# Kernel tuning notes

Measured on AMD Instinct MI355X. Metric: run time of the kernel, lower is better.

The kernel has to match this reference:

```python
import jax, jax.numpy as jnp
import numpy as np

NEG_SLOPE = 0.2
NUM_GRAPHS = 64


def _gat_layer(x, src, dst, W, att_src, att_dst, bias, concat):
    # x: [N, Fin]; W: [Fin, H*C]; att_*: [H, C]; bias: [H*C] or [C]
    N = x.shape[0]
    H, C = att_src.shape
    h = (x @ W).reshape(N, H, C)                      # per-head projections
    a_src = jnp.sum(h * att_src, axis=-1)             # [N, H]
    a_dst = jnp.sum(h * att_dst, axis=-1)             # [N, H]
    e = jax.nn.leaky_relu(a_src[src] + a_dst[dst], NEG_SLOPE)  # [E, H]
    # segment softmax over incoming edges per destination node
    m = jnp.full((N, H), -jnp.inf, dtype=e.dtype).at[dst].max(e)
    p = jnp.exp(e - m[dst])                           # [E, H]
    denom = jnp.zeros((N, H), dtype=e.dtype).at[dst].add(p)
    alpha = p / denom[dst]                            # [E, H]
    msg = h[src] * alpha[:, :, None]                  # [E, H, C]
    out = jnp.zeros((N, H, C), dtype=h.dtype).at[dst].add(msg)
    out = out.reshape(N, H * C) if concat else out.mean(axis=1)
    return out + bias


def _with_self_loops(edge_index, n):
    loop = jnp.arange(n, dtype=edge_index.dtype)
    src = jnp.concatenate([edge_index[0], loop])
    dst = jnp.concatenate([edge_index[1], loop])
    return src, dst


def setup_inputs() -> dict:
    key = jax.random.key(0)
    ks = jax.random.split(key, 12)
    N, E, Fin, C, H, A = 50000, 800000, 128, 64, 4, 32
    HC = H * C
    x = jax.random.normal(ks[0], (N, Fin), dtype=jnp.float32)
    edge_index = jax.random.randint(ks[1], (2, E), 0, N, dtype=jnp.int64)
    batch = jnp.sort(jax.random.randint(ks[2], (N,), 0, NUM_GRAPHS, dtype=jnp.int64))
    s1 = 1.0 / np.sqrt(Fin)
    s2 = 1.0 / np.sqrt(HC)
    return {
        "x": x,
        "edge_index": edge_index,
        "batch": batch,
        "num_wires": 8,
        "num_terminals": 8,
        "W1": jax.random.normal(ks[3], (Fin, HC), dtype=jnp.float32) * s1,
        "att_src1": jax.random.normal(ks[4], (H, C), dtype=jnp.float32) * s1,
        "att_dst1": jax.random.normal(ks[5], (H, C), dtype=jnp.float32) * s1,
        "b1": jnp.zeros((HC,), dtype=jnp.float32),
        "W2": jax.random.normal(ks[6], (HC, HC), dtype=jnp.float32) * s2,
        "att_src2": jax.random.normal(ks[7], (H, C), dtype=jnp.float32) * s2,
        "att_dst2": jax.random.normal(ks[8], (H, C), dtype=jnp.float32) * s2,
        "b2": jnp.zeros((C,), dtype=jnp.float32),
        "Wa": jax.random.normal(ks[9], (C, A), dtype=jnp.float32) * (1.0 / np.sqrt(C)),
        "ba": jnp.zeros((A,), dtype=jnp.float32),
    }


def reference(x, edge_index, batch, num_wires, num_terminals,
              W1, att_src1, att_dst1, b1, W2, att_src2, att_dst2, b2, Wa, ba):
    N = x.shape[0]
    src, dst = _with_self_loops(edge_index, N)
    h = jax.nn.elu(_gat_layer(x, src, dst, W1, att_src1, att_dst1, b1, concat=True))
    h = jax.nn.elu(_gat_layer(h, src, dst, W2, att_src2, att_dst2, b2, concat=False))
    # global mean pool per graph
    sums = jax.ops.segment_sum(h, batch, num_segments=NUM_GRAPHS)
    cnts = jax.ops.segment_sum(jnp.ones((N,), dtype=h.dtype), batch, num_segments=NUM_GRAPHS)
    pooled = sums / jnp.maximum(cnts, 1.0)[:, None]   # [G, C]
    return pooled @ Wa + ba                            # [G, num_actions]
```

## Files before the change

### kernel.cpp

```cpp
#include <hip/hip_runtime.h>
#include <hip/hip_bf16.h>
#include <cstdint>
#include <cstddef>

#define FIN      128
#define HGAT_H   4
#define HGAT_C   64
#define HGAT_HC  256
#define NGRAPHS  64
#define NACT     32
#define LOG2E    1.4426950408889634f

typedef unsigned int   uint32;
typedef unsigned short ushort_t;

using short8 = __attribute__((ext_vector_type(8))) short;
using u16x8  = __attribute__((ext_vector_type(8))) ushort_t;
using f32x4  = __attribute__((ext_vector_type(4))) float;
using f32x2  = __attribute__((ext_vector_type(2))) float;

__device__ __forceinline__ float bf2f(ushort_t u) {
    return __uint_as_float(((uint32)u) << 16);
}
__device__ __forceinline__ float bflo(uint32 q) {
    return __uint_as_float(q << 16);
}
__device__ __forceinline__ float bfhi(uint32 q) {
    return __uint_as_float(q & 0xFFFF0000u);
}
__device__ __forceinline__ ushort_t f2bf(float f) {
    __hip_bfloat16 h = __float2bfloat16(f);
    return *reinterpret_cast<ushort_t*>(&h);
}

__device__ __forceinline__ void att_fold_one(
    const float* __restrict__ W, const float* __restrict__ as,
    const float* __restrict__ ad, ushort_t* __restrict__ attBt,
    int K, int idx)
{
    const int k = idx >> 3, j = idx & 7;
    const int h = j >> 1;
    const float* av = (j & 1) ? ad : as;
    float s = 0.f;
#pragma unroll 8
    for (int c = 0; c < HGAT_C; ++c)
        s += W[(size_t)k * HGAT_HC + h * 64 + c] * av[h * 64 + c];
    const ushort_t hi = f2bf(s);
    const float    lo = s - bf2f(hi);
    attBt[(size_t)j * K + k]       = hi;
    attBt[(size_t)(j + 8) * K + k] = f2bf(lo);
}

#define CNT_BLOCKS 128

__global__ __launch_bounds__(256) void bucket_count_prep_kernel(
    const int* __restrict__ ei, int* __restrict__ bcnt,
    const float* __restrict__ W1, const float* __restrict__ W2,
    const float* __restrict__ as1, const float* __restrict__ ad1,
    const float* __restrict__ as2, const float* __restrict__ ad2,
    ushort_t* __restrict__ Wt1, ushort_t* __restrict__ Wt2,
    ushort_t* __restrict__ attBt1, ushort_t* __restrict__ attBt2, int E)
{
    const int t = threadIdx.x;
    if (blockIdx.x < CNT_BLOCKS) {
        __shared__ int hist[256];
        hist[t] = 0;
        __syncthreads();
        const int chunk = (E + CNT_BLOCKS - 1) / CNT_BLOCKS;
        const int lo = blockIdx.x * chunk;
        const int hi = min(lo + chunk, E);
        for (int e = lo + t; e < hi; e += 256)
            atomicAdd(&hist[ei[E + e] >> 8], 1);
        __syncthreads();
        if (hist[t] > 0) atomicAdd(&bcnt[t], hist[t]);
        return;
    }
    const int idx = (blockIdx.x - CNT_BLOCKS) * 256 + t;
    const int n1 = FIN * HGAT_HC;
    const int n2 = HGAT_HC * HGAT_HC;
    if (idx < n1) {
        const int k = idx >> 8, c = idx & 255;
        Wt1[(size_t)c * FIN + k] = f2bf(W1[idx]);
    } else if (idx < n1 + n2) {
        const int j = idx - n1;
        const int k = j >> 8, c = j & 255;
        Wt2[(size_t)c * HGAT_HC + k] = f2bf(W2[j]);
    } else if (idx < n1 + n2 + FIN * 8) {
        att_fold_one(W1, as1, ad1, attBt1, FIN, idx - n1 - n2);
    } else if (idx < n1 + n2 + (FIN + HGAT_HC) * 8) {
        att_fold_one(W2, as2, ad2, attBt2, HGAT_HC, idx - n1 - n2 - FIN * 8);
    }
}

__global__ __launch_bounds__(256) void bucket_scan_kernel(
    const int* __restrict__ bcnt, int* __restrict__ boff,
    int* __restrict__ bcur)
{
    __shared__ int sm[256];
    const int t = threadIdx.x;
    const int v = bcnt[t];
    sm[t] = v;
    __syncthreads();
#pragma unroll
    for (int off = 1; off < 256; off <<= 1) {
        const int u = (t >= off) ? sm[t - off] : 0;
        __syncthreads();
        sm[t] += u;
        __syncthreads();
    }
    const int ex = sm[t] - v;
    boff[t] = ex;
    bcur[t] = ex;
    if (t == 255) boff[256] = sm[255];
}

__global__ __launch_bounds__(256) void bucket_scatter_kernel(
    const int* __restrict__ ei, int* __restrict__ bcur,
    int2* __restrict__ staging, int E)
{
    __shared__ int hist[256];
    __shared__ int base[256];
    __shared__ int cur[256];
    const int t = threadIdx.x;
    hist[t] = 0;
    __syncthreads();

    const int chunk = 4096;
    const int lo = blockIdx.x * chunk;
    const int hi = min(lo + chunk, E);

    for (int e = lo + t; e < hi; e += 256)
        atomicAdd(&hist[ei[E + e] >> 8], 1);
    __syncthreads();
    if (hist[t] > 0) base[t] = atomicAdd(&bcur[t], hist[t]);
    cur[t] = 0;
    __syncthreads();

    for (int e = lo + t; e < hi; e += 256) {
        const int s = ei[e];
        const int d = ei[E + e];
        const int b = d >> 8;
        const int r = atomicAdd(&cur[b], 1);
        staging[base[b] + r] = make_int2(s, d);
    }
}

__global__ __launch_bounds__(256) void bucket_fill_kernel(
    const int2* __restrict__ staging, const int* __restrict__ boff,
    int* __restrict__ rowptr, int* __restrict__ colsrc, int N, int E)
{
    __shared__ int deg[256];
    __shared__ int ssc[256];
    __shared__ int cur[256];
    const int t  = threadIdx.x;
    const int b  = blockIdx.x;
    const int lo = boff[b];
    const int hi = boff[b + 1];

    deg[t] = 0;
    __syncthreads();
    for (int e = lo + t; e < hi; e += 256)
        atomicAdd(&deg[staging[e].y & 255], 1);
    __syncthreads();

    const int v = deg[t];
    ssc[t] = v;
    __syncthreads();
#pragma unroll
    for (int off = 1; off < 256; off <<= 1) {
        const int u = (t >= off) ? ssc[t - off] : 0;
        __syncthreads();
        ssc[t] += u;
        __syncthreads();
    }
    const int pre  = ssc[t] - v;
    const int node = b * 256 + t;
    if (node < N) rowptr[node] = lo + pre;
    cur[t] = lo + pre;
    if (b == 0 && t == 0) rowptr[N] = E;
    __syncthreads();

    for (int e = lo + t; e < hi; e += 256) {
        const int2 sd = staging[e];
        const int pos = atomicAdd(&cur[sd.y & 255], 1);
        colsrc[pos] = sd.x;
    }
}

template <int K, bool AF32>
__global__ __launch_bounds__(256) void gemm_mfma_att_kernel(
    const void* __restrict__ Av, const ushort_t* __restrict__ Bt,
    const ushort_t* __restrict__ attBt, ushort_t* __restrict__ Cb,
    float* __restrict__ a_src, float* __restrict__ a_dst, int M)
{
    constexpr int KK   = K / 32;
    constexpr int NPF  = K / 32;
    constexpr int BSTR = K + 8;
    constexpr int CSTR = 72;
    __shared__ ushort_t Bs[64 * BSTR];
    __shared__ ushort_t AttS[16 * BSTR];
    __shared__ ushort_t Cs[64 * CSTR];

    const int t  = threadIdx.x;
    const int w  = t >> 6;
    const int l  = t & 63;
    const int lg = l >> 4;
    const int lr = l & 15;
    const int rowbase = blockIdx.x * 64 + w * 16;

    const int srow  = t & 63;
    const int cbase = (t >> 6) * (K / 4);

    short8 af[KK];
    {
        const int arow = rowbase + lr;
        const int gr   = arow < M ? arow : M - 1;
        if (AF32) {
            const float* Ap = (const float*)Av + (size_t)gr * K;
#pragma unroll
            for (int kk = 0; kk < KK; ++kk) {
                const float4 v0 = *reinterpret_cast<const float4*>(Ap + kk * 32 + lg * 8);
                const float4 v1 = *reinterpret_cast<const float4*>(Ap + kk * 32 + lg * 8 + 4);
                short8 s;
                s[0] = (short)f2bf(v0.x); s[1] = (short)f2bf(v0.y);
                s[2] = (short)f2bf(v0.z); s[3] = (short)f2bf(v0.w);
                s[4] = (short)f2bf(v1.x); s[5] = (short)f2bf(v1.y);
                s[6] = (short)f2bf(v1.z); s[7] = (short)f2bf(v1.w);
                af[kk] = s;
            }
        } else {
            const ushort_t* Ap = (const ushort_t*)Av + (size_t)gr * K;
#pragma unroll
            for (int kk = 0; kk < KK; ++kk)
                af[kk] = *reinterpret_cast<const short8*>(Ap + kk * 32 + lg * 8);
        }
    }

    {
        const int r  = t & 15;
        const int cb = (t >> 4) * (K / 16);
        const ushort_t* src = attBt + (size_t)r * K + cb;
        ushort_t*       dst = &AttS[r * BSTR + cb];
#pragma unroll
        for (int j = 0; j < K / 128; ++j)
            *reinterpret_cast<u16x8*>(dst + j * 8) =
                *reinterpret_cast<const u16x8*>(src + j * 8);
    }
    {
        const ushort_t* src = Bt + (size_t)srow * K + cbase;
        ushort_t*       dst = &Bs[srow * BSTR + cbase];
#pragma unroll
        for (int j = 0; j < NPF; ++j)
            *reinterpret_cast<u16x8*>(dst + j * 8) =
                *reinterpret_cast<const u16x8*>(src + j * 8);
    }
    __syncthreads();

    {
        f32x4 aacc = {0.f, 0.f, 0.f, 0.f};
#pragma unroll
        for (int kk = 0; kk < KK; ++kk) {
            const short8 bfr = *reinterpret_cast<const short8*>(
                &AttS[lr * BSTR + kk * 32 + lg * 8]);
            aacc = __builtin_amdgcn_mfma_f32_16x16x32_bf16(af[kk], bfr, aacc, 0, 0, 0);
        }
#pragma unroll
        for (int reg = 0; reg < 4; ++reg) {
            const int gm = rowbase + lg * 4 + reg;
            const float v = aacc[reg] + __shfl_xor(aacc[reg], 8);
            if (lr < 8 && gm < M) {
                const int hh = lr >> 1;
                if (lr & 1) a_dst[gm * 4 + hh] = v * LOG2E;
                else        a_src[gm * 4 + hh] = v * LOG2E;
            }
        }
    }

    u16x8 pf[NPF];
#pragma unroll
    for (int head = 0; head < HGAT_H; ++head) {
        if (head < HGAT_H - 1) {
            const ushort_t* src =
                Bt + ((size_t)(head + 1) * 64 + srow) * K + cbase;
#pragma unroll
            for (int j = 0; j < NPF; ++j)
                pf[j] = *reinterpret_cast<const u16x8*>(src + j * 8);
        }

        f32x4 acc[4];
#pragma unroll
        for (int ct = 0; ct < 4; ++ct) acc[ct] = {0.f, 0.f, 0.f, 0.f};

#pragma unroll
        for (int kk = 0; kk < KK; ++kk) {
            short8 bfr[4];
#pragma unroll
            for (int ct = 0; ct < 4; ++ct)
                bfr[ct] = *reinterpret_cast<const short8*>(
                    &Bs[(ct * 16 + lr) * BSTR + kk * 32 + lg * 8]);
#pragma unroll
            for (int ct = 0; ct < 4; ++ct)
                acc[ct] = __builtin_amdgcn_mfma_f32_16x16x32_bf16(
                    af[kk], bfr[ct], acc[ct], 0, 0, 0);
        }

#pragma unroll
        for (int reg = 0; reg < 4; ++reg) {
            const int r = w * 16 + lg * 4 + reg;
#pragma unroll
            for (int ct = 0; ct < 4; ++ct)
                Cs[r * CSTR + ct * 16 + lr] = f2bf(acc[ct][reg]);
        }
        __syncthreads();

        const int n0 = head * 64;
        {
            const int cc = (t & 7) * 8;
#pragma unroll
            for (int it = 0; it < 2; ++it) {
                const int r  = (t >> 3) + it * 32;
                const int gm = blockIdx.x * 64 + r;
                if (gm < M) {
                    const u16x8 val = *reinterpret_cast<const u16x8*>(&Cs[r * CSTR + cc]);
                    *reinterpret_cast<u16x8*>(&Cb[(size_t)gm * HGAT_HC + n0 + cc]) = val;
                }
            }
        }

        if (head < HGAT_H - 1) {
            ushort_t* dst = &Bs[srow * BSTR + cbase];
#pragma unroll
            for (int j = 0; j < NPF; ++j)
                *reinterpret_cast<u16x8*>(dst + j * 8) = pf[j];
        }
        __syncthreads();
    }
}

template <int MODE>
__global__ __launch_bounds__(256) void aggregate_csr_kernel(
    const int* __restrict__ rowptr, const int* __restrict__ colsrc,
    const ushort_t* __restrict__ hb, const float* __restrict__ a_src,
    const float* __restrict__ a_dst, const float* __restrict__ bias,
    ushort_t* __restrict__ out, int N)
{
    const int wave = (blockIdx.x * 256 + threadIdx.x) >> 6;
    const int lane = threadIdx.x & 63;
    const int half = lane >> 5;
    const int hl   = lane & 31;
    const int d    = wave * 2 + half;
    if (d >= N) return;

    const int c0 = hl * 8;
    const int h  = hl >> 3;
    const float ad = a_dst[d * 4 + h];

    f32x2 a01 = {0.f, 0.f}, a23 = {0.f, 0.f}, a45 = {0.f, 0.f}, a67 = {0.f, 0.f};
    float den = 0.f;

    const int beg = rowptr[d], end = rowptr[d + 1];
    int i = beg;
    for (; i + 4 <= end; i += 4) {
        int   sv[4];
        float av[4];
        uint4 qv[4];
#pragma unroll
        for (int j = 0; j < 4; ++j) sv[j] = colsrc[i + j];
#pragma unroll
        for (int j = 0; j < 4; ++j) av[j] = a_src[sv[j] * 4 + h];
#pragma unroll
        for (int j = 0; j < 4; ++j)
            qv[j] = *reinterpret_cast<const uint4*>(&hb[(size_t)sv[j] * HGAT_HC + c0]);
#pragma unroll
        for (int j = 0; j < 4; ++j) {
            float ee = av[j] + ad;
            ee = fmaxf(ee, 0.2f * ee);
            const float wgt = __builtin_amdgcn_exp2f(ee);
            const f32x2 w2 = {wgt, wgt};
            a01 += w2 * f32x2{bflo(qv[j].x), bfhi(qv[j].x)};
            a23 += w2 * f32x2{bflo(qv[j].y), bfhi(qv[j].y)};
            a45 += w2 * f32x2{bflo(qv[j].z), bfhi(qv[j].z)};
            a67 += w2 * f32x2{bflo(qv[j].w), bfhi(qv[j].w)};
            den += wgt;
        }
    }
    for (; i < end; ++i) {
        const int s = colsrc[i];
        float ee = a_src[s * 4 + h] + ad;
        ee = fmaxf(ee, 0.2f * ee);
        const float wgt = __builtin_amdgcn_exp2f(ee);
        const uint4 q = *reinterpret_cast<const uint4*>(&hb[(size_t)s * HGAT_HC + c0]);
        const f32x2 w2 = {wgt, wgt};
        a01 += w2 * f32x2{bflo(q.x), bfhi(q.x)};
        a23 += w2 * f32x2{bflo(q.y), bfhi(q.y)};
        a45 += w2 * f32x2{bflo(q.z), bfhi(q.z)};
        a67 += w2 * f32x2{bflo(q.w), bfhi(q.w)};
        den += wgt;
    }
    {
        float ee = a_src[d * 4 + h] + ad;
        ee = fmaxf(ee, 0.2f * ee);
        const float wgt = __builtin_amdgcn_exp2f(ee);
        const uint4 q = *reinterpret_cast<const uint4*>(&hb[(size_t)d * HGAT_HC + c0]);
        const f32x2 w2 = {wgt, wgt};
        a01 += w2 * f32x2{bflo(q.x), bfhi(q.x)};
        a23 += w2 * f32x2{bflo(q.y), bfhi(q.y)};
        a45 += w2 * f32x2{bflo(q.z), bfhi(q.z)};
        a67 += w2 * f32x2{bflo(q.w), bfhi(q.w)};
        den += wgt;
    }

    const float inv = 1.0f / den;
    float v[8] = {a01.x * inv, a01.y * inv, a23.x * inv, a23.y * inv,
                  a45.x * inv, a45.y * inv, a67.x * inv, a67.y * inv};

    if (MODE == 0) {
        const float4 b0 = *reinterpret_cast<const float4*>(&bias[c0]);
        const float4 b1 = *reinterpret_cast<const float4*>(&bias[c0 + 4]);
        v[0] += b0.x; v[1] += b0.y; v[2] += b0.z; v[3] += b0.w;
        v[4] += b1.x; v[5] += b1.y; v[6] += b1.z; v[7] += b1.w;
        u16x8 u;
#pragma unroll
        for (int j = 0; j < 8; ++j) {
            const float r = v[j] > 0.f ? v[j] : expm1f(v[j]);
            u[j] = f2bf(r);
        }
        *reinterpret_cast<u16x8*>(&out[(size_t)d * HGAT_HC + c0]) = u;
    } else {
#pragma unroll
        for (int j = 0; j < 8; ++j) {
            v[j] += __shfl_xor(v[j], 8);
            v[j] += __shfl_xor(v[j], 16);
        }
        if (hl < 8) {
            const int c = hl * 8;
            const float4 b0 = *reinterpret_cast<const float4*>(&bias[c]);
            const float4 b1 = *reinterpret_cast<const float4*>(&bias[c + 4]);
            const float bb[8] = {b0.x, b0.y, b0.z, b0.w, b1.x, b1.y, b1.z, b1.w};
            u16x8 u;
#pragma unroll
            for (int j = 0; j < 8; ++j) {
                float r = 0.25f * v[j] + bb[j];
                r = r > 0.f ? r : expm1f(r);
                u[j] = f2bf(r);
            }
            *reinterpret_cast<u16x8*>(&out[(size_t)d * HGAT_C + c]) = u;
        }
    }
}

__device__ __forceinline__ int lower_bound_batch(
    const int* __restrict__ batch, int N, int key)
{
    int lo = 0, hi = N;
    while (lo < hi) {
        const int mid = (lo + hi) >> 1;
        if (batch[mid] < key) lo = mid + 1; else hi = mid;
    }
    return lo;
}

__global__ __launch_bounds__(256) void pool_partial_kernel(
    const ushort_t* __restrict__ hfin, const int* __restrict__ batch,
    float* __restrict__ partial, int N)
{
    const int g   = blockIdx.x >> 3;
    const int s   = blockIdx.x & 7;
    const int t   = threadIdx.x;
    const int c   = t & 63;
    const int sub = t >> 6;

    const int beg = lower_bound_batch(batch, N, g);
    const int end = lower_bound_batch(batch, N, g + 1);
    const int len = end - beg;
    const int sl  = (len + 7) >> 3;
    const int sb  = beg + s * sl;
    const int se  = sb + sl < end ? sb + sl : end;

    float acc = 0.f;
    for (int n = sb + sub; n < se; n += 4)
        acc += bf2f(hfin[(size_t)n * HGAT_C + c]);

    __shared__ float sm[256];
    sm[t] = acc;
    __syncthreads();
    if (sub == 0)
        partial[(size_t)(g * 8 + s) * HGAT_C + c] =
            sm[c] + sm[64 + c] + sm[128 + c] + sm[192 + c];
}

__global__ __launch_bounds__(64) void pool_final_fused_kernel(
    const float* __restrict__ partial, const int* __restrict__ batch,
    const float* __restrict__ Wa, const float* __restrict__ ba,
    float* __restrict__ out, int N)
{
    const int g = blockIdx.x;
    const int c = threadIdx.x;
    const int beg = lower_bound_batch(batch, N, g);
    const int end = lower_bound_batch(batch, N, g + 1);
    float s = 0.f;
#pragma unroll
    for (int k = 0; k < 8; ++k)
        s += partial[(size_t)(g * 8 + k) * HGAT_C + c];
    s /= fmaxf((float)(end - beg), 1.0f);

    __shared__ float pr[HGAT_C];
    pr[c] = s;
    __syncthreads();
    if (c < NACT) {
        float o = ba[c];
#pragma unroll
        for (int cc = 0; cc < HGAT_C; ++cc)
            o += pr[cc] * Wa[cc * NACT + c];
        out[g * NACT + c] = o;
    }
}

extern "C" void kernel_launch(void* const* d_in, const int* in_sizes, int n_in,
                              void* d_out, int out_size, void* d_ws, size_t ws_size,
                              hipStream_t stream)
{
    const float* x     = (const float*)d_in[0];
    const int*   ei    = (const int*)d_in[1];
    const int*   batch = (const int*)d_in[2];
    const float* W1    = (const float*)d_in[5];
    const float* as1   = (const float*)d_in[6];
    const float* ad1   = (const float*)d_in[7];
    const float* b1    = (const float*)d_in[8];
    const float* W2    = (const float*)d_in[9];
    const float* as2   = (const float*)d_in[10];
    const float* ad2   = (const float*)d_in[11];
    const float* b2    = (const float*)d_in[12];
    const float* Wa    = (const float*)d_in[13];
    const float* ba    = (const float*)d_in[14];

    const int N = in_sizes[0] / FIN;
    const int E = in_sizes[1] / 2;

    char* ws = (char*)d_ws;
    size_t off = 0;
    auto alloc = [&](size_t bytes) -> void* {
        void* p = ws + off;
        off += (bytes + 255) & ~(size_t)255;
        return p;
    };
    ushort_t* hb      = (ushort_t*)alloc((size_t)N * HGAT_HC * 2);
    ushort_t* hpost   = (ushort_t*)alloc((size_t)N * HGAT_HC * 2);
    ushort_t* Wt1     = (ushort_t*)alloc((size_t)FIN * HGAT_HC * 2);
    ushort_t* Wt2     = (ushort_t*)alloc((size_t)HGAT_HC * HGAT_HC * 2);
    ushort_t* attBt1  = (ushort_t*)alloc((size_t)16 * FIN * 2);
    ushort_t* attBt2  = (ushort_t*)alloc((size_t)16 * HGAT_HC * 2);
    float*    a_src   = (float*)alloc((size_t)N * 4 * 4);
    float*    a_dst   = (float*)alloc((size_t)N * 4 * 4);
    int*      rowptr  = (int*)alloc((size_t)(N + 1) * 4);
    int*      colsrc  = (int*)alloc((size_t)E * 4);
    int2*     staging = (int2*)alloc((size_t)E * 8);
    int*      bcnt    = (int*)alloc(256 * 4);
    int*      boff    = (int*)alloc(257 * 4);
    int*      bcur    = (int*)alloc(256 * 4);
    float*    partial = (float*)alloc((size_t)NGRAPHS * 8 * HGAT_C * 4);
    ushort_t* hfin    = hpost;
    (void)ws_size; (void)n_in; (void)out_size;

    const int gemmBlocks = (N + 63) / 64;
    const int aggBlocks  = (N + 7) / 8;
    const int NBKT       = (N + 255) >> 8;
    const int prepTot    = FIN * HGAT_HC + HGAT_HC * HGAT_HC + (FIN + HGAT_HC) * 8;
    const int prepBlocks = (prepTot + 255) / 256;

    hipMemsetAsync(bcnt, 0, 256 * 4, stream);
    bucket_count_prep_kernel<<<CNT_BLOCKS + prepBlocks, 256, 0, stream>>>(
        ei, bcnt, W1, W2, as1, ad1, as2, ad2, Wt1, Wt2, attBt1, attBt2, E);
    bucket_scan_kernel<<<1, 256, 0, stream>>>(bcnt, boff, bcur);
    bucket_scatter_kernel<<<(E + 4095) / 4096, 256, 0, stream>>>(
        ei, bcur, staging, E);
    bucket_fill_kernel<<<NBKT, 256, 0, stream>>>(
        staging, boff, rowptr, colsrc, N, E);

    gemm_mfma_att_kernel<FIN, true><<<gemmBlocks, 256, 0, stream>>>(
        x, Wt1, attBt1, hb, a_src, a_dst, N);
    aggregate_csr_kernel<0><<<aggBlocks, 256, 0, stream>>>(
        rowptr, colsrc, hb, a_src, a_dst, b1, hpost, N);

    gemm_mfma_att_kernel<HGAT_HC, false><<<gemmBlocks, 256, 0, stream>>>(
        hpost, Wt2, attBt2, hb, a_src, a_dst, N);
    aggregate_csr_kernel<1><<<aggBlocks, 256, 0, stream>>>(
        rowptr, colsrc, hb, a_src, a_dst, b2, hfin, N);

    pool_partial_kernel<<<NGRAPHS * 8, 256, 0, stream>>>(hfin, batch, partial, N);
    pool_final_fused_kernel<<<NGRAPHS, 64, 0, stream>>>(
        partial, batch, Wa, ba, (float*)d_out, N);
}
```

Baseline: 238.9 us.

## Fuse edge scatter with first GEMM launch and replace atomic bucket count

Each counting block now writes its own 256-bin histogram to a per-block array, and the scan kernel reduces those in a loop. This removes the memset and the global atomics. The bucket scatter and the first-layer projection GEMM are merged into one launch with block-index dispatch, so the memory-bound scatter blocks can run alongside the MFMA GEMM blocks and one launch is saved. The cost is a serial 128-step reduction per thread in the scan kernel. The fused kernel's shared memory and register use is set by the larger GEMM body, which can limit how many scatter blocks fit per CU.

Result: faster. 225.8 us (median of 2 runs) (-5.5%).

```diff
diff --git a/kernel.cpp b/kernel.cpp
--- a/kernel.cpp
+++ b/kernel.cpp
@@ -10,6 +10,7 @@
 #define NGRAPHS  64
 #define NACT     32
 #define LOG2E    1.4426950408889634f
+#define CNT_BLOCKS 128
 
 typedef unsigned int   uint32;
 typedef unsigned short ushort_t;
@@ -51,10 +52,8 @@
     attBt[(size_t)(j + 8) * K + k] = f2bf(lo);
 }
 
-#define CNT_BLOCKS 128
-
 __global__ __launch_bounds__(256) void bucket_count_prep_kernel(
-    const int* __restrict__ ei, int* __restrict__ bcnt,
+    const int* __restrict__ ei, int* __restrict__ bhist,
     const float* __restrict__ W1, const float* __restrict__ W2,
     const float* __restrict__ as1, const float* __restrict__ ad1,
     const float* __restrict__ as2, const float* __restrict__ ad2,
@@ -72,7 +71,7 @@
         for (int e = lo + t; e < hi; e += 256)
             atomicAdd(&hist[ei[E + e] >> 8], 1);
         __syncthreads();
-        if (hist[t] > 0) atomicAdd(&bcnt[t], hist[t]);
+        bhist[blockIdx.x * 256 + t] = hist[t];
         return;
     }
     const int idx = (blockIdx.x - CNT_BLOCKS) * 256 + t;
@@ -93,12 +92,13 @@
 }
 
 __global__ __launch_bounds__(256) void bucket_scan_kernel(
-    const int* __restrict__ bcnt, int* __restrict__ boff,
+    const int* __restrict__ bhist, int* __restrict__ boff,
     int* __restrict__ bcur)
 {
     __shared__ int sm[256];
     const int t = threadIdx.x;
-    const int v = bcnt[t];
+    int v = 0;
+    for (int j = 0; j < CNT_BLOCKS; ++j) v += bhist[j * 256 + t];
     sm[t] = v;
     __syncthreads();
 #pragma unroll
@@ -114,9 +114,9 @@
     if (t == 255) boff[256] = sm[255];
 }
 
-__global__ __launch_bounds__(256) void bucket_scatter_kernel(
+__device__ __forceinline__ void scatter_body(
     const int* __restrict__ ei, int* __restrict__ bcur,
-    int2* __restrict__ staging, int E)
+    int2* __restrict__ staging, int E, int blk)
 {
     __shared__ int hist[256];
     __shared__ int base[256];
@@ -126,7 +126,7 @@
     __syncthreads();
 
     const int chunk = 4096;
-    const int lo = blockIdx.x * chunk;
+    const int lo = blk * chunk;
     const int hi = min(lo + chunk, E);
 
     for (int e = lo + t; e < hi; e += 256)
@@ -188,10 +188,10 @@
 }
 
 template <int K, bool AF32>
-__global__ __launch_bounds__(256) void gemm_mfma_att_kernel(
+__device__ __forceinline__ void gemm_body(
     const void* __restrict__ Av, const ushort_t* __restrict__ Bt,
     const ushort_t* __restrict__ attBt, ushort_t* __restrict__ Cb,
-    float* __restrict__ a_src, float* __restrict__ a_dst, int M)
+    float* __restrict__ a_src, float* __restrict__ a_dst, int M, int blk)
 {
     constexpr int KK   = K / 32;
     constexpr int NPF  = K / 32;
@@ -206,7 +206,7 @@
     const int l  = t & 63;
     const int lg = l >> 4;
     const int lr = l & 15;
-    const int rowbase = blockIdx.x * 64 + w * 16;
+    const int rowbase = blk * 64 + w * 16;
 
     const int srow  = t & 63;
     const int cbase = (t >> 6) * (K / 4);
@@ -319,7 +319,7 @@
 #pragma unroll
             for (int it = 0; it < 2; ++it) {
                 const int r  = (t >> 3) + it * 32;
-                const int gm = blockIdx.x * 64 + r;
+                const int gm = blk * 64 + r;
                 if (gm < M) {
                     const u16x8 val = *reinterpret_cast<const u16x8*>(&Cs[r * CSTR + cc]);
                     *reinterpret_cast<u16x8*>(&Cb[(size_t)gm * HGAT_HC + n0 + cc]) = val;
@@ -335,6 +335,29 @@
         }
         __syncthreads();
     }
+}
+
+__global__ __launch_bounds__(256) void scatter_gemm1_kernel(
+    const int* __restrict__ ei, int* __restrict__ bcur,
+    int2* __restrict__ staging, int E, int SB,
+    const float* __restrict__ x, const ushort_t* __restrict__ Wt1,
+    const ushort_t* __restrict__ attBt1, ushort_t* __restrict__ hb,
+    float* __restrict__ a_src, float* __restrict__ a_dst, int M)
+{
+    if ((int)blockIdx.x < SB) {
+        scatter_body(ei, bcur, staging, E, blockIdx.x);
+        return;
+    }
+    gemm_body<FIN, true>(x, Wt1, attBt1, hb, a_src, a_dst, M,
+                         blockIdx.x - SB);
+}
+
+__global__ __launch_bounds__(256) void gemm2_kernel(
+    const ushort_t* __restrict__ A, const ushort_t* __restrict__ Wt2,
+    const ushort_t* __restrict__ attBt2, ushort_t* __restrict__ hb,
+    float* __restrict__ a_src, float* __restrict__ a_dst, int M)
+{
+    gemm_body<HGAT_HC, false>(A, Wt2, attBt2, hb, a_src, a_dst, M, blockIdx.x);
 }
 
 template <int MODE>
@@ -555,7 +578,7 @@
     int*      rowptr  = (int*)alloc((size_t)(N + 1) * 4);
     int*      colsrc  = (int*)alloc((size_t)E * 4);
     int2*     staging = (int2*)alloc((size_t)E * 8);
-    int*      bcnt    = (int*)alloc(256 * 4);
+    int*      bhist   = (int*)alloc((size_t)CNT_BLOCKS * 256 * 4);
     int*      boff    = (int*)alloc(257 * 4);
     int*      bcur    = (int*)alloc(256 * 4);
     float*    partial = (float*)alloc((size_t)NGRAPHS * 8 * HGAT_C * 4);
@@ -565,24 +588,25 @@
     const int gemmBlocks = (N + 63) / 64;
     const int aggBlocks  = (N + 7) / 8;
     const int NBKT       = (N + 255) >> 8;
+    const int SB         = (E + 4095) / 4096;
     const int prepTot    = FIN * HGAT_HC + HGAT_HC * HGAT_HC + (FIN + HGAT_HC) * 8;
     const int prepBlocks = (prepTot + 255) / 256;
 
-    hipMemsetAsync(bcnt, 0, 256 * 4, stream);
     bucket_count_prep_kernel<<<CNT_BLOCKS + prepBlocks, 256, 0, stream>>>(
-        ei, bcnt, W1, W2, as1, ad1, as2, ad2, Wt1, Wt2, attBt1, attBt2, E);
-    bucket_scan_kernel<<<1, 256, 0, stream>>>(bcnt, boff, bcur);
-    bucket_scatter_kernel<<<(E + 4095) / 4096, 256, 0, stream>>>(
-        ei, bcur, staging, E);
+        ei, bhist, W1, W2, as1, ad1, as2, ad2, Wt1, Wt2, attBt1, attBt2, E);
+
+    bucket_scan_kernel<<<1, 256, 0, stream>>>(bhist, boff, bcur);
+
+    scatter_gemm1_kernel<<<SB + gemmBlocks, 256, 0, stream>>>(
+        ei, bcur, staging, E, SB, x, Wt1, attBt1, hb, a_src, a_dst, N);
+
     bucket_fill_kernel<<<NBKT, 256, 0, stream>>>(
         staging, boff, rowptr, colsrc, N, E);
 
-    gemm_mfma_att_kernel<FIN, true><<<gemmBlocks, 256, 0, stream>>>(
-        x, Wt1, attBt1, hb, a_src, a_dst, N);
     aggregate_csr_kernel<0><<<aggBlocks, 256, 0, stream>>>(
         rowptr, colsrc, hb, a_src, a_dst, b1, hpost, N);
 
-    gemm_mfma_att_kernel<HGAT_HC, false><<<gemmBlocks, 256, 0, stream>>>(
+    gemm2_kernel<<<gemmBlocks, 256, 0, stream>>>(
         hpost, Wt2, attBt2, hb, a_src, a_dst, N);
     aggregate_csr_kernel<1><<<aggBlocks, 256, 0, stream>>>(
         rowptr, colsrc, hb, a_src, a_dst, b2, hfin, N);
```
